# Kernel optimization log

Measured on AMD Instinct MI355X. Metric: run time of the kernel, lower is better.

Reference implementation:

```python
import jax, jax.numpy as jnp
import numpy as np

N, IN_DIM, MLPW, HID, NCLS = 2048, 1024, 16, 256, 4


def setup_inputs() -> dict:
    key = jax.random.key(0)
    ks = jax.random.split(key, 12)
    f32 = jnp.float32
    return {
        "x": jax.random.normal(ks[0], (N, IN_DIM), f32),
        "adj": jax.random.uniform(ks[1], (N, N), f32),
        "xdeg": jax.random.uniform(ks[2], (N, N), f32),
        "ydeg": jax.random.uniform(ks[3], (N, N), f32),
        # edge MLP([3, mlp_width, 2])
        "Wm1": jax.random.normal(ks[4], (3, MLPW), f32) * (1.0 / np.sqrt(3.0)),
        "bm1": jnp.zeros((MLPW,), f32),
        "Wm2": jax.random.normal(ks[5], (MLPW, 2), f32) * (1.0 / np.sqrt(MLPW)),
        "bm2": jnp.zeros((2,), f32),
        # GCN / dense layers (stored as [in, out]; torch Linear applies x @ W.T)
        "Wg1": jax.random.normal(ks[6], (IN_DIM, HID), f32) * (1.0 / np.sqrt(IN_DIM)),
        "Wl2": jax.random.normal(ks[7], (HID, 64), f32) * (1.0 / np.sqrt(HID)),
        "bl2": jnp.zeros((64,), f32),
        "Wg2": jax.random.normal(ks[8], (64, NCLS), f32) * (1.0 / 8.0),
    }


def reference(x, adj, xdeg, ydeg, Wm1, bm1, Wm2, bm2, Wg1, Wl2, bl2, Wg2):
    n = adj.shape[0]
    # Edge-feature MLP mask. The torch code gathers nonzero entries, runs the
    # MLP, scatters back into a zero buffer, then multiplies by adj. Computing
    # the mask densely is mathematically identical because adj * mask is zero
    # wherever adj is zero.
    feats = jnp.stack([adj, xdeg, ydeg], axis=-1)          # [N, N, 3]
    h = jax.nn.relu(feats @ Wm1 + bm1)                     # [N, N, MLPW]
    mask = jax.nn.softmax(h @ Wm2 + bm2, axis=-1)[..., 1]  # [N, N]
    A = adj * mask + jnp.eye(n, dtype=adj.dtype)
    # Symmetric-ish normalization: D_row^{-1/2} A D_col^{-1/2}
    # (the torch diag-matmul chain reduces to this row/col scaling).
    rowsum = jnp.sum(A, axis=1)
    colsum = jnp.sum(A, axis=0)
    dr = jnp.where(rowsum > 0, jax.lax.rsqrt(jnp.where(rowsum > 0, rowsum, 1.0)), 0.0)
    dc = jnp.where(colsum > 0, jax.lax.rsqrt(jnp.where(colsum > 0, colsum, 1.0)), 0.0)
    A = dr[:, None] * A * dc[None, :]
    # GCN layer 1 (dropout = identity in eval mode)
    hid = (A @ (x @ Wg1)) @ Wl2 + bl2                      # [N, 64]
    # GCN layer 2
    out = A @ (hid @ Wg2)                                  # [N, n_classes]
    return out, hid
```

## Files before the change

kernel.cpp:

```cpp
#include <hip/hip_runtime.h>

#define NN 2048
#define MLPW 16

typedef __attribute__((ext_vector_type(8))) short short8v;
typedef __attribute__((ext_vector_type(16))) float float16v;
typedef __attribute__((ext_vector_type(4))) unsigned short ushort4v;
typedef __attribute__((ext_vector_type(8))) unsigned short ushort8v;

__device__ __forceinline__ unsigned short f2b(float f) {
  unsigned int u = __float_as_uint(f);
  unsigned int r = (u + 0x7fffu + ((u >> 16) & 1u)) >> 16;
  return (unsigned short)r;
}
__device__ __forceinline__ float b2f(unsigned short u) {
  return __uint_as_float(((unsigned int)u) << 16);
}

__global__ void __launch_bounds__(256) edge_kernel(
    const float* __restrict__ adj, const float* __restrict__ xdeg,
    const float* __restrict__ ydeg,
    const float* __restrict__ Wm1, const float* __restrict__ bm1,
    const float* __restrict__ Wm2, const float* __restrict__ bm2,
    const float* __restrict__ x, const float* __restrict__ Wg1,
    unsigned short* __restrict__ Abf, float* __restrict__ dr,
    unsigned short* __restrict__ xb, unsigned short* __restrict__ Wg1T) {
  const int tid = threadIdx.x;
  const int b = blockIdx.x;
  if (b >= 3072) {
    const int bo = b - 3072;
    const int n = bo * 2 + (tid >> 7);
    const int k0 = (tid & 127) * 8;
    ushort8v o;
#pragma unroll
    for (int e = 0; e < 8; e++) o[e] = f2b(Wg1[(size_t)(k0 + e) * 256 + n]);
    *(ushort8v*)&Wg1T[(size_t)n * 1024 + k0] = o;
    return;
  }
  if (b >= 2048) {
    const size_t idx = (size_t)(b - 2048) * 2048 + (size_t)tid * 8;
    const float4 u = *(const float4*)&x[idx], v = *(const float4*)&x[idx + 4];
    ushort8v o = {f2b(u.x), f2b(u.y), f2b(u.z), f2b(u.w),
                  f2b(v.x), f2b(v.y), f2b(v.z), f2b(v.w)};
    *(ushort8v*)&xb[idx] = o;
    return;
  }
  __shared__ float w1[48], b1[16], w2[32], b2s[2];
  __shared__ float wsum[4];
  if (tid < 48) w1[tid] = Wm1[tid];
  if (tid < 16) b1[tid] = bm1[tid];
  if (tid < 32) w2[tid] = Wm2[tid];
  if (tid < 2) b2s[tid] = bm2[tid];
  __syncthreads();
  const int i = b;
  const float4* adj4 = (const float4*)(adj + (size_t)i * NN);
  const float4* xd4 = (const float4*)(xdeg + (size_t)i * NN);
  const float4* yd4 = (const float4*)(ydeg + (size_t)i * NN);
  ushort4v* A4 = (ushort4v*)(Abf + (size_t)i * NN);
  float rsum = 0.f;
  for (int j4 = tid; j4 < NN / 4; j4 += 256) {
    float4 av = adj4[j4], xv = xd4[j4], yv = yd4[j4];
    float aa[4] = {av.x, av.y, av.z, av.w};
    float xx[4] = {xv.x, xv.y, xv.z, xv.w};
    float yy[4] = {yv.x, yv.y, yv.z, yv.w};
    ushort4v oo;
#pragma unroll
    for (int e = 0; e < 4; e++) {
      float l0 = b2s[0], l1 = b2s[1];
#pragma unroll
      for (int k = 0; k < MLPW; k++) {
        float h = fmaf(aa[e], w1[k], fmaf(xx[e], w1[16 + k], fmaf(yy[e], w1[32 + k], b1[k])));
        h = fmaxf(h, 0.f);
        l0 = fmaf(h, w2[2 * k], l0);
        l1 = fmaf(h, w2[2 * k + 1], l1);
      }
      float mask = 1.f / (1.f + __expf(l0 - l1));
      float v = aa[e] * mask;
      int j = j4 * 4 + e;
      if (j == i) v += 1.f;
      oo[e] = f2b(v);
      rsum += v;
    }
    A4[j4] = oo;
  }
#pragma unroll
  for (int off = 32; off > 0; off >>= 1) rsum += __shfl_down(rsum, off);
  if ((tid & 63) == 0) wsum[tid >> 6] = rsum;
  __syncthreads();
  if (tid == 0) {
    float t = wsum[0] + wsum[1] + wsum[2] + wsum[3];
    dr[i] = t > 0.f ? rsqrtf(t) : 0.f;
  }
}

__global__ void __launch_bounds__(256) dc_kernel(
    const unsigned short* __restrict__ Abf, float* __restrict__ dc) {
  __shared__ float part[64][32];
  const int tid = threadIdx.x;
  const int c0 = blockIdx.x * 32;
  const int cA = (tid & 3) * 8, rgA = tid >> 2;
  float sa[8] = {0, 0, 0, 0, 0, 0, 0, 0};
  const unsigned short* ap = Abf + (size_t)rgA * NN + c0 + cA;
#pragma unroll 4
  for (int k = 0; k < 32; k++) {
    ushort8v u = *(const ushort8v*)ap;
#pragma unroll
    for (int e = 0; e < 8; e++) sa[e] += b2f(u[e]);
    ap += (size_t)64 * NN;
  }
#pragma unroll
  for (int e = 0; e < 8; e++) part[rgA][cA + e] = sa[e];
  __syncthreads();
  if (tid < 32) {
    float d = 0.f;
#pragma unroll
    for (int rg = 0; rg < 64; rg++) d += part[rg][tid];
    dc[c0 + tid] = d > 0.f ? rsqrtf(d) : 0.f;
  }
}

__global__ void __launch_bounds__(256) gemm1_kernel(
    const unsigned short* __restrict__ A, const unsigned short* __restrict__ B,
    const float* __restrict__ dc, unsigned short* __restrict__ XWT) {
  constexpr int SW = 136;
  __shared__ unsigned short As[64 * SW];
  __shared__ unsigned short Bs[64 * SW];
  const int tid = threadIdx.x;
  const int lane = tid & 63, wave = tid >> 6;
  const int l31 = lane & 31, half = lane >> 5;
  const int mh = wave & 1, nh = wave >> 1;
  const int row0 = blockIdx.y * 64, col0 = blockIdx.x * 64;

  float16v acc;
#pragma unroll
  for (int r = 0; r < 16; r++) acc[r] = 0.f;

  for (int k0 = 0; k0 < 1024; k0 += 128) {
#pragma unroll
    for (int i = 0; i < 4; i++) {
      const int id = tid + i * 256;
      const int r = id >> 4, c = id & 15;
      *(ushort8v*)&As[r * SW + c * 8] =
          *(const ushort8v*)&A[(size_t)(row0 + r) * 1024 + k0 + c * 8];
      *(ushort8v*)&Bs[r * SW + c * 8] =
          *(const ushort8v*)&B[(size_t)(col0 + r) * 1024 + k0 + c * 8];
    }
    __syncthreads();
#pragma unroll
    for (int ks = 0; ks < 8; ks++) {
      short8v a = *(const short8v*)&As[(mh * 32 + l31) * SW + ks * 16 + half * 8];
      short8v b = *(const short8v*)&Bs[(nh * 32 + l31) * SW + ks * 16 + half * 8];
      acc = __builtin_amdgcn_mfma_f32_32x32x16_bf16(a, b, acc, 0, 0, 0);
    }
    __syncthreads();
  }
  const int n = col0 + nh * 32 + l31;
  const float dv = dc[n];
  unsigned short* Xb = XWT + (size_t)(row0 + mh * 32) * NN + n;
#pragma unroll
  for (int reg = 0; reg < 16; reg++) {
    const int m = (reg & 3) + 8 * (reg >> 2) + 4 * half;
    Xb[(size_t)m * NN] = f2b(acc[reg] * dv);
  }
}

__global__ void __launch_bounds__(256) gemm_splitk_kernel(
    const unsigned short* __restrict__ A, const unsigned short* __restrict__ B,
    float* __restrict__ P, int M, int N, int K, int Kc) {
  constexpr int SW = 136;
  __shared__ unsigned short As[64 * SW];
  __shared__ unsigned short Bs[128 * SW];
  const int tid = threadIdx.x;
  const int lane = tid & 63, wave = tid >> 6;
  const int l31 = lane & 31, half = lane >> 5;
  const int mh = wave & 1, nh = wave >> 1;
  const int row0 = blockIdx.y * 64, col0 = blockIdx.x * 128;
  const int kbeg = blockIdx.z * Kc;

  float16v acc0, acc1;
#pragma unroll
  for (int r = 0; r < 16; r++) { acc0[r] = 0.f; acc1[r] = 0.f; }

  for (int k0 = 0; k0 < Kc; k0 += 128) {
#pragma unroll
    for (int i = 0; i < 4; i++) {
      const int id = tid + i * 256;
      const int r = id >> 4, c = id & 15;
      *(ushort8v*)&As[r * SW + c * 8] =
          *(const ushort8v*)&A[(size_t)(row0 + r) * K + kbeg + k0 + c * 8];
    }
#pragma unroll
    for (int i = 0; i < 8; i++) {
      const int id = tid + i * 256;
      const int r = id >> 4, c = id & 15;
      *(ushort8v*)&Bs[r * SW + c * 8] =
          *(const ushort8v*)&B[(size_t)(col0 + r) * K + kbeg + k0 + c * 8];
    }
    __syncthreads();
#pragma unroll
    for (int ks = 0; ks < 8; ks++) {
      short8v a = *(const short8v*)&As[(mh * 32 + l31) * SW + ks * 16 + half * 8];
      short8v b0 = *(const short8v*)&Bs[(nh * 64 + l31) * SW + ks * 16 + half * 8];
      short8v b1 = *(const short8v*)&Bs[(nh * 64 + 32 + l31) * SW + ks * 16 + half * 8];
      acc0 = __builtin_amdgcn_mfma_f32_32x32x16_bf16(a, b0, acc0, 0, 0, 0);
      acc1 = __builtin_amdgcn_mfma_f32_32x32x16_bf16(a, b1, acc1, 0, 0, 0);
    }
    __syncthreads();
  }
  float* Pb = P + ((size_t)blockIdx.z * M + row0 + mh * 32) * N + col0 + nh * 64 + l31;
#pragma unroll
  for (int reg = 0; reg < 16; reg++) {
    const int m = (reg & 3) + 8 * (reg >> 2) + 4 * half;
    Pb[(size_t)m * N] = acc0[reg];
    Pb[(size_t)m * N + 32] = acc1[reg];
  }
}

__global__ void __launch_bounds__(256) tail_kernel(
    const float* __restrict__ P2, const float* __restrict__ dr,
    const float* __restrict__ dc, const float* __restrict__ Wl2,
    const float* __restrict__ bl2, const float* __restrict__ Wg2,
    float* __restrict__ hid, float* __restrict__ HW) {
  __shared__ float T1s[8][256];
  __shared__ float hidS[8][68];
  const int m0 = blockIdx.x * 8;
  const int tid = threadIdx.x;
#pragma unroll
  for (int i = 0; i < 8; i++) {
    const int idx = tid + i * 256;
    const int mi = idx >> 8, n = idx & 255;
    float s = 0.f;
#pragma unroll
    for (int sk = 0; sk < 8; sk++)
      s += P2[((size_t)sk * 2048 + m0 + mi) * 256 + n];
    T1s[mi][n] = s * dr[m0 + mi];
  }
  __syncthreads();
  const int j = tid & 63, mg = tid >> 6;
  float h0 = bl2[j], h1 = h0;
#pragma unroll 8
  for (int n = 0; n < 256; n++) {
    float w = Wl2[(size_t)n * 64 + j];
    h0 = fmaf(T1s[mg * 2 + 0][n], w, h0);
    h1 = fmaf(T1s[mg * 2 + 1][n], w, h1);
  }
  hid[(size_t)(m0 + mg * 2 + 0) * 64 + j] = h0;
  hid[(size_t)(m0 + mg * 2 + 1) * 64 + j] = h1;
  hidS[mg * 2 + 0][j] = h0;
  hidS[mg * 2 + 1][j] = h1;
  __syncthreads();
  if (tid < 32) {
    const int r = tid >> 2, c = tid & 3;
    float s = 0.f;
#pragma unroll
    for (int jj = 0; jj < 64; jj++) s = fmaf(hidS[r][jj], Wg2[jj * 4 + c], s);
    HW[(size_t)(m0 + r) * 4 + c] = s * dc[m0 + r];
  }
}

__global__ void __launch_bounds__(256) out_kernel(
    const unsigned short* __restrict__ Abf, const float* __restrict__ HW,
    const float* __restrict__ dr, float* __restrict__ outp) {
  const int i = blockIdx.x, tid = threadIdx.x;
  const ushort8v a8 = ((const ushort8v*)(Abf + (size_t)i * NN))[tid];
  const float4* hw4 = (const float4*)HW;
  const int j0 = tid * 8;
  float ax = 0.f, ay = 0.f, az = 0.f, aw = 0.f;
#pragma unroll
  for (int e = 0; e < 8; e++) {
    float a = b2f(a8[e]);
    float4 h = hw4[j0 + e];
    ax = fmaf(a, h.x, ax);
    ay = fmaf(a, h.y, ay);
    az = fmaf(a, h.z, az);
    aw = fmaf(a, h.w, aw);
  }
#pragma unroll
  for (int off = 32; off > 0; off >>= 1) {
    ax += __shfl_down(ax, off);
    ay += __shfl_down(ay, off);
    az += __shfl_down(az, off);
    aw += __shfl_down(aw, off);
  }
  __shared__ float wsum[4][4];
  const int w = tid >> 6;
  if ((tid & 63) == 0) {
    wsum[w][0] = ax; wsum[w][1] = ay; wsum[w][2] = az; wsum[w][3] = aw;
  }
  __syncthreads();
  if (tid < 4)
    outp[(size_t)i * 4 + tid] =
        dr[i] * (wsum[0][tid] + wsum[1][tid] + wsum[2][tid] + wsum[3][tid]);
}

extern "C" void kernel_launch(void* const* d_in, const int* in_sizes, int n_in,
                              void* d_out, int out_size, void* d_ws, size_t ws_size,
                              hipStream_t stream) {
  const float* x    = (const float*)d_in[0];
  const float* adj  = (const float*)d_in[1];
  const float* xdeg = (const float*)d_in[2];
  const float* ydeg = (const float*)d_in[3];
  const float* Wm1  = (const float*)d_in[4];
  const float* bm1  = (const float*)d_in[5];
  const float* Wm2  = (const float*)d_in[6];
  const float* bm2  = (const float*)d_in[7];
  const float* Wg1  = (const float*)d_in[8];
  const float* Wl2  = (const float*)d_in[9];
  const float* bl2  = (const float*)d_in[10];
  const float* Wg2  = (const float*)d_in[11];

  char* ws = (char*)d_ws;
  unsigned short* Abf  = (unsigned short*)(ws);
  unsigned short* xb   = (unsigned short*)(ws + 8388608);
  unsigned short* Wg1T = (unsigned short*)(ws + 12582912);
  unsigned short* XWT  = (unsigned short*)(ws + 13107200);
  float* P2   = (float*)(ws + 14155776);
  float* dr   = (float*)(ws + 30932992);
  float* dc   = (float*)(ws + 30941184);
  float* HW   = (float*)(ws + 30949376);

  float* outp = (float*)d_out;
  float* hid  = (float*)d_out + 2048 * 4;

  edge_kernel<<<3200, 256, 0, stream>>>(adj, xdeg, ydeg, Wm1, bm1, Wm2, bm2,
                                        x, Wg1, Abf, dr, xb, Wg1T);
  dc_kernel<<<64, 256, 0, stream>>>(Abf, dc);
  gemm1_kernel<<<dim3(2048 / 64, 256 / 64), 256, 0, stream>>>(Wg1T, xb, dc, XWT);
  gemm_splitk_kernel<<<dim3(256 / 128, 2048 / 64, 8), 256, 0, stream>>>(
      Abf, XWT, P2, 2048, 256, 2048, 256);
  tail_kernel<<<2048 / 8, 256, 0, stream>>>(P2, dr, dc, Wl2, bl2, Wg2, hid, HW);
  out_kernel<<<NN, 256, 0, stream>>>(Abf, HW, dr, outp);
}
```

Baseline: 168.7 us.

## Fuse post-edge kernels into one cooperative persistent kernel with grid syncs

Merges the dc, gemm1, split-K GEMM, tail and output kernels into a single cooperative kernel of 512 blocks, using grid.sync() between stages. The column-sum and the first GEMM now run at the same time in disjoint block ranges, and the GEMM result is held in registers across the sync before being scaled by dc. This removes four kernel launch gaps and tail effects. In exchange it adds grid-wide barrier costs, requires 512 co-resident blocks, and gives the output stage less parallelism (4 rows per block).

```diff
diff --git a/kernel.cpp b/kernel.cpp
--- a/kernel.cpp
+++ b/kernel.cpp
@@ -1,4 +1,7 @@
 #include <hip/hip_runtime.h>
+#include <hip/hip_cooperative_groups.h>
+
+namespace cg = cooperative_groups;
 
 #define NN 2048
 #define MLPW 16
@@ -93,204 +96,210 @@
   }
 }
 
-__global__ void __launch_bounds__(256) dc_kernel(
-    const unsigned short* __restrict__ Abf, float* __restrict__ dc) {
-  __shared__ float part[64][32];
+__global__ void __launch_bounds__(256, 2) mega_kernel(
+    const unsigned short* __restrict__ Abf, const unsigned short* __restrict__ xb,
+    const unsigned short* __restrict__ Wg1T, const float* __restrict__ dr,
+    float* __restrict__ dc, unsigned short* __restrict__ XWT,
+    float* __restrict__ P2, const float* __restrict__ Wl2,
+    const float* __restrict__ bl2, const float* __restrict__ Wg2,
+    float* __restrict__ hid, float* __restrict__ HW, float* __restrict__ outp) {
+  cg::grid_group grid = cg::this_grid();
+  __shared__ __align__(16) unsigned char smem[52224];
+  constexpr int SW = 136;
   const int tid = threadIdx.x;
-  const int c0 = blockIdx.x * 32;
-  const int cA = (tid & 3) * 8, rgA = tid >> 2;
-  float sa[8] = {0, 0, 0, 0, 0, 0, 0, 0};
-  const unsigned short* ap = Abf + (size_t)rgA * NN + c0 + cA;
-#pragma unroll 4
-  for (int k = 0; k < 32; k++) {
-    ushort8v u = *(const ushort8v*)ap;
-#pragma unroll
-    for (int e = 0; e < 8; e++) sa[e] += b2f(u[e]);
-    ap += (size_t)64 * NN;
-  }
-#pragma unroll
-  for (int e = 0; e < 8; e++) part[rgA][cA + e] = sa[e];
-  __syncthreads();
-  if (tid < 32) {
-    float d = 0.f;
-#pragma unroll
-    for (int rg = 0; rg < 64; rg++) d += part[rg][tid];
-    dc[c0 + tid] = d > 0.f ? rsqrtf(d) : 0.f;
-  }
-}
-
-__global__ void __launch_bounds__(256) gemm1_kernel(
-    const unsigned short* __restrict__ A, const unsigned short* __restrict__ B,
-    const float* __restrict__ dc, unsigned short* __restrict__ XWT) {
-  constexpr int SW = 136;
-  __shared__ unsigned short As[64 * SW];
-  __shared__ unsigned short Bs[64 * SW];
-  const int tid = threadIdx.x;
+  const int bid = blockIdx.x;
   const int lane = tid & 63, wave = tid >> 6;
   const int l31 = lane & 31, half = lane >> 5;
-  const int mh = wave & 1, nh = wave >> 1;
-  const int row0 = blockIdx.y * 64, col0 = blockIdx.x * 64;
-
-  float16v acc;
-#pragma unroll
-  for (int r = 0; r < 16; r++) acc[r] = 0.f;
-
-  for (int k0 = 0; k0 < 1024; k0 += 128) {
-#pragma unroll
-    for (int i = 0; i < 4; i++) {
-      const int id = tid + i * 256;
-      const int r = id >> 4, c = id & 15;
-      *(ushort8v*)&As[r * SW + c * 8] =
-          *(const ushort8v*)&A[(size_t)(row0 + r) * 1024 + k0 + c * 8];
-      *(ushort8v*)&Bs[r * SW + c * 8] =
-          *(const ushort8v*)&B[(size_t)(col0 + r) * 1024 + k0 + c * 8];
-    }
+
+  float16v acc1;
+#pragma unroll
+  for (int r = 0; r < 16; r++) acc1[r] = 0.f;
+
+  if (bid < 64) {
+    float(*part)[32] = (float(*)[32])smem;
+    const int c0 = bid * 32;
+    const int cA = (tid & 3) * 8, rgA = tid >> 2;
+    float sa[8] = {0, 0, 0, 0, 0, 0, 0, 0};
+    const unsigned short* ap = Abf + (size_t)rgA * NN + c0 + cA;
+#pragma unroll 4
+    for (int k = 0; k < 32; k++) {
+      ushort8v u = *(const ushort8v*)ap;
+#pragma unroll
+      for (int e = 0; e < 8; e++) sa[e] += b2f(u[e]);
+      ap += (size_t)64 * NN;
+    }
+#pragma unroll
+    for (int e = 0; e < 8; e++) part[rgA][cA + e] = sa[e];
     __syncthreads();
-#pragma unroll
-    for (int ks = 0; ks < 8; ks++) {
-      short8v a = *(const short8v*)&As[(mh * 32 + l31) * SW + ks * 16 + half * 8];
-      short8v b = *(const short8v*)&Bs[(nh * 32 + l31) * SW + ks * 16 + half * 8];
-      acc = __builtin_amdgcn_mfma_f32_32x32x16_bf16(a, b, acc, 0, 0, 0);
+    if (tid < 32) {
+      float d = 0.f;
+#pragma unroll
+      for (int rg = 0; rg < 64; rg++) d += part[rg][tid];
+      dc[c0 + tid] = d > 0.f ? rsqrtf(d) : 0.f;
+    }
+  } else if (bid < 192) {
+    unsigned short* As = (unsigned short*)smem;
+    unsigned short* Bs = (unsigned short*)(smem + 17408);
+    const int g = bid - 64;
+    const int row0 = (g >> 5) * 64, col0 = (g & 31) * 64;
+    const int mh = wave & 1, nh = wave >> 1;
+    for (int k0 = 0; k0 < 1024; k0 += 128) {
+#pragma unroll
+      for (int i = 0; i < 4; i++) {
+        const int id = tid + i * 256;
+        const int r = id >> 4, c = id & 15;
+        *(ushort8v*)&As[r * SW + c * 8] =
+            *(const ushort8v*)&Wg1T[(size_t)(row0 + r) * 1024 + k0 + c * 8];
+        *(ushort8v*)&Bs[r * SW + c * 8] =
+            *(const ushort8v*)&xb[(size_t)(col0 + r) * 1024 + k0 + c * 8];
+      }
+      __syncthreads();
+#pragma unroll
+      for (int ks = 0; ks < 8; ks++) {
+        short8v a = *(const short8v*)&As[(mh * 32 + l31) * SW + ks * 16 + half * 8];
+        short8v b = *(const short8v*)&Bs[(nh * 32 + l31) * SW + ks * 16 + half * 8];
+        acc1 = __builtin_amdgcn_mfma_f32_32x32x16_bf16(a, b, acc1, 0, 0, 0);
+      }
+      __syncthreads();
+    }
+  }
+  grid.sync();
+
+  if (bid >= 64 && bid < 192) {
+    const int g = bid - 64;
+    const int row0 = (g >> 5) * 64, col0 = (g & 31) * 64;
+    const int mh = wave & 1, nh = wave >> 1;
+    const int n = col0 + nh * 32 + l31;
+    const float dv = dc[n];
+    unsigned short* Xb = XWT + (size_t)(row0 + mh * 32) * NN + n;
+#pragma unroll
+    for (int reg = 0; reg < 16; reg++) {
+      const int m = (reg & 3) + 8 * (reg >> 2) + 4 * half;
+      Xb[(size_t)m * NN] = f2b(acc1[reg] * dv);
+    }
+  }
+  grid.sync();
+
+  {
+    unsigned short* As = (unsigned short*)smem;
+    unsigned short* Bs = (unsigned short*)(smem + 17408);
+    const int sk = bid >> 6;
+    const int by = (bid & 63) >> 1, bx = bid & 1;
+    const int row0 = by * 64, col0 = bx * 128;
+    const int kbeg = sk * 256;
+    const int mh = wave & 1, nh = wave >> 1;
+    float16v acc0, accb;
+#pragma unroll
+    for (int r = 0; r < 16; r++) { acc0[r] = 0.f; accb[r] = 0.f; }
+    for (int k0 = 0; k0 < 256; k0 += 128) {
+#pragma unroll
+      for (int i = 0; i < 4; i++) {
+        const int id = tid + i * 256;
+        const int r = id >> 4, c = id & 15;
+        *(ushort8v*)&As[r * SW + c * 8] =
+            *(const ushort8v*)&Abf[(size_t)(row0 + r) * NN + kbeg + k0 + c * 8];
+      }
+#pragma unroll
+      for (int i = 0; i < 8; i++) {
+        const int id = tid + i * 256;
+        const int r = id >> 4, c = id & 15;
+        *(ushort8v*)&Bs[r * SW + c * 8] =
+            *(const ushort8v*)&XWT[(size_t)(col0 + r) * NN + kbeg + k0 + c * 8];
+      }
+      __syncthreads();
+#pragma unroll
+      for (int ks = 0; ks < 8; ks++) {
+        short8v a = *(const short8v*)&As[(mh * 32 + l31) * SW + ks * 16 + half * 8];
+        short8v b0 = *(const short8v*)&Bs[(nh * 64 + l31) * SW + ks * 16 + half * 8];
+        short8v b1 = *(const short8v*)&Bs[(nh * 64 + 32 + l31) * SW + ks * 16 + half * 8];
+        acc0 = __builtin_amdgcn_mfma_f32_32x32x16_bf16(a, b0, acc0, 0, 0, 0);
+        accb = __builtin_amdgcn_mfma_f32_32x32x16_bf16(a, b1, accb, 0, 0, 0);
+      }
+      __syncthreads();
+    }
+    float* Pb = P2 + ((size_t)sk * 2048 + row0 + mh * 32) * 256 + col0 + nh * 64 + l31;
+#pragma unroll
+    for (int reg = 0; reg < 16; reg++) {
+      const int m = (reg & 3) + 8 * (reg >> 2) + 4 * half;
+      Pb[(size_t)m * 256] = acc0[reg];
+      Pb[(size_t)m * 256 + 32] = accb[reg];
+    }
+  }
+  grid.sync();
+
+  if (bid < 256) {
+    float(*T1s)[256] = (float(*)[256])smem;
+    float(*hidS)[68] = (float(*)[68])(smem + 8192);
+    const int m0 = bid * 8;
+#pragma unroll
+    for (int i = 0; i < 8; i++) {
+      const int idx = tid + i * 256;
+      const int mi = idx >> 8, n = idx & 255;
+      float s = 0.f;
+#pragma unroll
+      for (int sk = 0; sk < 8; sk++)
+        s += P2[((size_t)sk * 2048 + m0 + mi) * 256 + n];
+      T1s[mi][n] = s * dr[m0 + mi];
     }
     __syncthreads();
-  }
-  const int n = col0 + nh * 32 + l31;
-  const float dv = dc[n];
-  unsigned short* Xb = XWT + (size_t)(row0 + mh * 32) * NN + n;
-#pragma unroll
-  for (int reg = 0; reg < 16; reg++) {
-    const int m = (reg & 3) + 8 * (reg >> 2) + 4 * half;
-    Xb[(size_t)m * NN] = f2b(acc[reg] * dv);
-  }
-}
-
-__global__ void __launch_bounds__(256) gemm_splitk_kernel(
-    const unsigned short* __restrict__ A, const unsigned short* __restrict__ B,
-    float* __restrict__ P, int M, int N, int K, int Kc) {
-  constexpr int SW = 136;
-  __shared__ unsigned short As[64 * SW];
-  __shared__ unsigned short Bs[128 * SW];
-  const int tid = threadIdx.x;
-  const int lane = tid & 63, wave = tid >> 6;
-  const int l31 = lane & 31, half = lane >> 5;
-  const int mh = wave & 1, nh = wave >> 1;
-  const int row0 = blockIdx.y * 64, col0 = blockIdx.x * 128;
-  const int kbeg = blockIdx.z * Kc;
-
-  float16v acc0, acc1;
-#pragma unroll
-  for (int r = 0; r < 16; r++) { acc0[r] = 0.f; acc1[r] = 0.f; }
-
-  for (int k0 = 0; k0 < Kc; k0 += 128) {
-#pragma unroll
-    for (int i = 0; i < 4; i++) {
-      const int id = tid + i * 256;
-      const int r = id >> 4, c = id & 15;
-      *(ushort8v*)&As[r * SW + c * 8] =
-          *(const ushort8v*)&A[(size_t)(row0 + r) * K + kbeg + k0 + c * 8];
-    }
-#pragma unroll
-    for (int i = 0; i < 8; i++) {
-      const int id = tid + i * 256;
-      const int r = id >> 4, c = id & 15;
-      *(ushort8v*)&Bs[r * SW + c * 8] =
-          *(const ushort8v*)&B[(size_t)(col0 + r) * K + kbeg + k0 + c * 8];
-    }
+    const int j = tid & 63, mg = tid >> 6;
+    float h0 = bl2[j], h1 = h0;
+#pragma unroll 8
+    for (int n = 0; n < 256; n++) {
+      float w = Wl2[(size_t)n * 64 + j];
+      h0 = fmaf(T1s[mg * 2 + 0][n], w, h0);
+      h1 = fmaf(T1s[mg * 2 + 1][n], w, h1);
+    }
+    hid[(size_t)(m0 + mg * 2 + 0) * 64 + j] = h0;
+    hid[(size_t)(m0 + mg * 2 + 1) * 64 + j] = h1;
+    hidS[mg * 2 + 0][j] = h0;
+    hidS[mg * 2 + 1][j] = h1;
     __syncthreads();
-#pragma unroll
-    for (int ks = 0; ks < 8; ks++) {
-      short8v a = *(const short8v*)&As[(mh * 32 + l31) * SW + ks * 16 + half * 8];
-      short8v b0 = *(const short8v*)&Bs[(nh * 64 + l31) * SW + ks * 16 + half * 8];
-      short8v b1 = *(const short8v*)&Bs[(nh * 64 + 32 + l31) * SW + ks * 16 + half * 8];
-      acc0 = __builtin_amdgcn_mfma_f32_32x32x16_bf16(a, b0, acc0, 0, 0, 0);
-      acc1 = __builtin_amdgcn_mfma_f32_32x32x16_bf16(a, b1, acc1, 0, 0, 0);
-    }
-    __syncthreads();
-  }
-  float* Pb = P + ((size_t)blockIdx.z * M + row0 + mh * 32) * N + col0 + nh * 64 + l31;
-#pragma unroll
-  for (int reg = 0; reg < 16; reg++) {
-    const int m = (reg & 3) + 8 * (reg >> 2) + 4 * half;
-    Pb[(size_t)m * N] = acc0[reg];
-    Pb[(size_t)m * N + 32] = acc1[reg];
-  }
-}
-
-__global__ void __launch_bounds__(256) tail_kernel(
-    const float* __restrict__ P2, const float* __restrict__ dr,
-    const float* __restrict__ dc, const float* __restrict__ Wl2,
-    const float* __restrict__ bl2, const float* __restrict__ Wg2,
-    float* __restrict__ hid, float* __restrict__ HW) {
-  __shared__ float T1s[8][256];
-  __shared__ float hidS[8][68];
-  const int m0 = blockIdx.x * 8;
-  const int tid = threadIdx.x;
-#pragma unroll
-  for (int i = 0; i < 8; i++) {
-    const int idx = tid + i * 256;
-    const int mi = idx >> 8, n = idx & 255;
-    float s = 0.f;
-#pragma unroll
-    for (int sk = 0; sk < 8; sk++)
-      s += P2[((size_t)sk * 2048 + m0 + mi) * 256 + n];
-    T1s[mi][n] = s * dr[m0 + mi];
-  }
-  __syncthreads();
-  const int j = tid & 63, mg = tid >> 6;
-  float h0 = bl2[j], h1 = h0;
-#pragma unroll 8
-  for (int n = 0; n < 256; n++) {
-    float w = Wl2[(size_t)n * 64 + j];
-    h0 = fmaf(T1s[mg * 2 + 0][n], w, h0);
-    h1 = fmaf(T1s[mg * 2 + 1][n], w, h1);
-  }
-  hid[(size_t)(m0 + mg * 2 + 0) * 64 + j] = h0;
-  hid[(size_t)(m0 + mg * 2 + 1) * 64 + j] = h1;
-  hidS[mg * 2 + 0][j] = h0;
-  hidS[mg * 2 + 1][j] = h1;
-  __syncthreads();
-  if (tid < 32) {
-    const int r = tid >> 2, c = tid & 3;
-    float s = 0.f;
-#pragma unroll
-    for (int jj = 0; jj < 64; jj++) s = fmaf(hidS[r][jj], Wg2[jj * 4 + c], s);
-    HW[(size_t)(m0 + r) * 4 + c] = s * dc[m0 + r];
-  }
-}
-
-__global__ void __launch_bounds__(256) out_kernel(
-    const unsigned short* __restrict__ Abf, const float* __restrict__ HW,
-    const float* __restrict__ dr, float* __restrict__ outp) {
-  const int i = blockIdx.x, tid = threadIdx.x;
-  const ushort8v a8 = ((const ushort8v*)(Abf + (size_t)i * NN))[tid];
-  const float4* hw4 = (const float4*)HW;
-  const int j0 = tid * 8;
-  float ax = 0.f, ay = 0.f, az = 0.f, aw = 0.f;
-#pragma unroll
-  for (int e = 0; e < 8; e++) {
-    float a = b2f(a8[e]);
-    float4 h = hw4[j0 + e];
-    ax = fmaf(a, h.x, ax);
-    ay = fmaf(a, h.y, ay);
-    az = fmaf(a, h.z, az);
-    aw = fmaf(a, h.w, aw);
-  }
-#pragma unroll
-  for (int off = 32; off > 0; off >>= 1) {
-    ax += __shfl_down(ax, off);
-    ay += __shfl_down(ay, off);
-    az += __shfl_down(az, off);
-    aw += __shfl_down(aw, off);
-  }
-  __shared__ float wsum[4][4];
-  const int w = tid >> 6;
-  if ((tid & 63) == 0) {
-    wsum[w][0] = ax; wsum[w][1] = ay; wsum[w][2] = az; wsum[w][3] = aw;
-  }
-  __syncthreads();
-  if (tid < 4)
-    outp[(size_t)i * 4 + tid] =
-        dr[i] * (wsum[0][tid] + wsum[1][tid] + wsum[2][tid] + wsum[3][tid]);
+    if (tid < 32) {
+      const int r = tid >> 2, c = tid & 3;
+      float s = 0.f;
+#pragma unroll
+      for (int jj = 0; jj < 64; jj++) s = fmaf(hidS[r][jj], Wg2[jj * 4 + c], s);
+      HW[(size_t)(m0 + r) * 4 + c] = s * dc[m0 + r];
+    }
+  }
+  grid.sync();
+
+  {
+    float(*wsum)[4] = (float(*)[4])smem;
+    const float4* hw4 = (const float4*)HW;
+    const int w = tid >> 6;
+    const int j0 = tid * 8;
+    for (int rr = 0; rr < 4; rr++) {
+      const int i = bid * 4 + rr;
+      const ushort8v a8 = ((const ushort8v*)(Abf + (size_t)i * NN))[tid];
+      float ax = 0.f, ay = 0.f, az = 0.f, aw = 0.f;
+#pragma unroll
+      for (int e = 0; e < 8; e++) {
+        float a = b2f(a8[e]);
+        float4 h = hw4[j0 + e];
+        ax = fmaf(a, h.x, ax);
+        ay = fmaf(a, h.y, ay);
+        az = fmaf(a, h.z, az);
+        aw = fmaf(a, h.w, aw);
+      }
+#pragma unroll
+      for (int off = 32; off > 0; off >>= 1) {
+        ax += __shfl_down(ax, off);
+        ay += __shfl_down(ay, off);
+        az += __shfl_down(az, off);
+        aw += __shfl_down(aw, off);
+      }
+      if ((tid & 63) == 0) {
+        wsum[w][0] = ax; wsum[w][1] = ay; wsum[w][2] = az; wsum[w][3] = aw;
+      }
+      __syncthreads();
+      if (tid < 4)
+        outp[(size_t)i * 4 + tid] =
+            dr[i] * (wsum[0][tid] + wsum[1][tid] + wsum[2][tid] + wsum[3][tid]);
+      __syncthreads();
+    }
+  }
 }
 
 extern "C" void kernel_launch(void* const* d_in, const int* in_sizes, int n_in,
@@ -324,10 +333,10 @@
 
   edge_kernel<<<3200, 256, 0, stream>>>(adj, xdeg, ydeg, Wm1, bm1, Wm2, bm2,
                                         x, Wg1, Abf, dr, xb, Wg1T);
-  dc_kernel<<<64, 256, 0, stream>>>(Abf, dc);
-  gemm1_kernel<<<dim3(2048 / 64, 256 / 64), 256, 0, stream>>>(Wg1T, xb, dc, XWT);
-  gemm_splitk_kernel<<<dim3(256 / 128, 2048 / 64, 8), 256, 0, stream>>>(
-      Abf, XWT, P2, 2048, 256, 2048, 256);
-  tail_kernel<<<2048 / 8, 256, 0, stream>>>(P2, dr, dc, Wl2, bl2, Wg2, hid, HW);
-  out_kernel<<<NN, 256, 0, stream>>>(Abf, HW, dr, outp);
-}
+  void* args[] = {(void*)&Abf, (void*)&xb, (void*)&Wg1T, (void*)&dr,
+                  (void*)&dc,  (void*)&XWT, (void*)&P2,  (void*)&Wl2,
+                  (void*)&bl2, (void*)&Wg2, (void*)&hid, (void*)&HW,
+                  (void*)&outp};
+  hipLaunchCooperativeKernel((const void*)mega_kernel, dim3(512), dim3(256),
+                             args, 0, stream);
+}
```

Result: slower. 390.7 us (+131.6%).
